# Performance work log

Measured on AMD Instinct MI355X. Metric: run time of the kernel, lower is better.

Reference implementation:

```python
import jax, jax.numpy as jnp
import numpy as np

B, D, HID, DC, K = 32768, 64, 512, 128, 12
CLAMP = 1.0
L1 = D // 2          # GLOW split lengths
L2 = D - L1
INIT = 0.01          # torch code rescales all params to 0.01*randn


def setup_inputs() -> dict:
    key = jax.random.key(0)
    ks = iter(jax.random.split(key, 16))
    # FrEIA PermuteRandom: np.random.seed(k); np.random.permutation(D)
    perms = jnp.asarray(
        np.stack([np.random.RandomState(k).permutation(D) for k in range(K)]),
        dtype=jnp.int32)
    f32 = jnp.float32
    return {
        'q_feat': jax.random.normal(next(ks), (B, 1, D), f32),
        'H': jax.random.normal(next(ks), (B, DC), f32),
        'perms': perms,
        'an_logscale': INIT * jax.random.normal(next(ks), (K, D), f32),
        'an_bias': INIT * jax.random.normal(next(ks), (K, D), f32),
        's1_W1': INIT * jax.random.normal(next(ks), (K, HID, L1 + DC), f32),
        's1_b1': INIT * jax.random.normal(next(ks), (K, HID), f32),
        's1_W2': INIT * jax.random.normal(next(ks), (K, 2 * L2, HID), f32),
        's1_b2': INIT * jax.random.normal(next(ks), (K, 2 * L2), f32),
        's2_W1': INIT * jax.random.normal(next(ks), (K, HID, L2 + DC), f32),
        's2_b1': INIT * jax.random.normal(next(ks), (K, HID), f32),
        's2_W2': INIT * jax.random.normal(next(ks), (K, 2 * L1, HID), f32),
        's2_b2': INIT * jax.random.normal(next(ks), (K, 2 * L1), f32),
    }


def _mlp(x, W1, b1, W2, b2):
    # torch Linear: y = x @ W.T + b
    h = jax.nn.relu(x @ W1.T + b1)
    return h @ W2.T + b2


def _log_e(s):
    # FrEIA GLOW soft clamp: log e(s) = clamp * 0.636 * atan(s / clamp)
    return CLAMP * 0.636 * jnp.arctan(s / CLAMP)


def reference(q_feat, H, perms, an_logscale, an_bias,
              s1_W1, s1_b1, s1_W2, s1_b2,
              s2_W1, s2_b1, s2_W2, s2_b2):
    x = q_feat.reshape(q_feat.shape[0], -1)          # Flatten: (B,1,D)->(B,D)
    logj = jnp.zeros(x.shape[0], x.dtype)

    def block(carry, p):
        x, logj = carry
        perm, ls, bi, w11, b11, w12, b12, w21, b21, w22, b22 = p
        x = x[:, perm]                               # PermuteRandom (logdet 0)
        x = x * jnp.exp(ls) + bi                     # ActNorm
        logj = logj + jnp.sum(ls)
        x1, x2 = x[:, :L1], x[:, L1:]                # GLOW coupling
        r2 = _mlp(jnp.concatenate([x2, H], 1), w21, b21, w22, b22)
        le2 = _log_e(r2[:, :L1])
        y1 = jnp.exp(le2) * x1 + r2[:, L1:]
        r1 = _mlp(jnp.concatenate([y1, H], 1), w11, b11, w12, b12)
        le1 = _log_e(r1[:, :L2])
        y2 = jnp.exp(le1) * x2 + r1[:, L2:]
        logj = logj + jnp.sum(le1, axis=1) + jnp.sum(le2, axis=1)
        return (jnp.concatenate([y1, y2], 1), logj), None

    (z, logj), _ = jax.lax.scan(
        block, (x, logj),
        (perms, an_logscale, an_bias,
         s1_W1, s1_b1, s1_W2, s1_b2,
         s2_W1, s2_b1, s2_W2, s2_b2))
    return z, logj
```

## Files before the change

### kernel.cpp

```cpp
#include <hip/hip_runtime.h>
#include <hip/hip_bf16.h>
#include <math.h>

#define B_ROWS 32768

typedef __attribute__((ext_vector_type(8)))  short        s8v;
typedef __attribute__((ext_vector_type(4)))  float        f4v;
typedef __attribute__((ext_vector_type(2)))  unsigned int u2v;
typedef __attribute__((ext_vector_type(4)))  unsigned int u4v;

__device__ __forceinline__ short f2bf(float f){
  unsigned u = __builtin_bit_cast(unsigned, f);
  u = (u + 0x7fffu + ((u >> 16) & 1u)) >> 16;
  return (short)u;
}
__device__ __forceinline__ unsigned cpk(float a, float b){
  __hip_bfloat16_raw lo = (__hip_bfloat16_raw)__float2bfloat16(a);
  __hip_bfloat16_raw hi = (__hip_bfloat16_raw)__float2bfloat16(b);
  return (unsigned)lo.x | ((unsigned)hi.x << 16);
}
__device__ __forceinline__ float bf_lo(unsigned u){ return __builtin_bit_cast(float, u << 16); }
__device__ __forceinline__ float bf_hi(unsigned u){ return __builtin_bit_cast(float, u & 0xffff0000u); }

#define MFMA16(A,B,C) __builtin_amdgcn_mfma_f32_16x16x32_bf16((A),(B),(C),0,0,0)

typedef __attribute__((address_space(1))) const unsigned int gu32;
typedef __attribute__((address_space(3))) unsigned int lu32;
__device__ __forceinline__ void gl_lds16(const unsigned short* g, char* l){
  __builtin_amdgcn_global_load_lds((gu32*)(const void*)g, (lu32*)(void*)l, 16, 0, 0);
}

#define OXFT 0
#define XFT_S 68
#define OXHB 17408
#define XHB_S 40
#define OHB  22528
#define HB_S 136
#define SL_S 68
#define SLOT_B 8704
#define OW1  39936
#define OLJ  80896
#define SM_SZ 81152

#define WF_W2 1966080
#define W_TOTAL 2752512

__global__ void cvtw_frag(const float* __restrict__ s1w1, const float* __restrict__ s1w2,
                          const float* __restrict__ s2w1, const float* __restrict__ s2w2,
                          unsigned short* __restrict__ dst)
{
  long t = (long)blockIdx.x * blockDim.x + threadIdx.x;
  if (t >= W_TOTAL) return;
  float v;
  if (t < WF_W2){
    int m = (int)(t / 81920); int r = (int)(t - (long)m*81920);
    int c = r / 20480;  int r2 = r - c*20480;
    int tile = r2 >> 9; int r3 = r2 & 511;
    int lane = r3 >> 3; int e = r3 & 7;
    int rg = tile / 5,  kk = tile - rg*5;
    int l15 = lane & 15, lq = lane >> 4;
    int h  = c*128 + rg*16 + l15;
    int ki = kk*32 + lq*8 + e;
    const float* src = (m & 1) ? s1w1 : s2w1;
    v = src[(size_t)(m >> 1)*81920 + h*160 + ki];
  } else {
    long u = t - WF_W2;
    int m = (int)(u / 32768); int r = (int)(u - (long)m*32768);
    int g = r >> 9; int r3 = r & 511;
    int lane = r3 >> 3; int e = r3 & 7;
    int c = g >> 4, hs = (g >> 2) & 3, ot = g & 3;
    int l15 = lane & 15, lq = lane >> 4;
    int o = ot*16 + l15;
    int h = c*128 + hs*32 + lq*8 + e;
    const float* src = (m & 1) ? s1w2 : s2w2;
    v = src[(size_t)(m >> 1)*32768 + o*512 + h];
  }
  dst[t] = (unsigned short)f2bf(v);
}

__global__ __launch_bounds__(256, 2) void cinn_dma(
    const float* __restrict__ q, const float* __restrict__ Hg,
    const int* __restrict__ perms,
    const float* __restrict__ ls_g, const float* __restrict__ bi_g,
    const float* __restrict__ s1b1, const float* __restrict__ s1b2,
    const float* __restrict__ s2b1, const float* __restrict__ s2b2,
    const unsigned short* __restrict__ wbf,
    float* __restrict__ outz, float* __restrict__ outlj)
{
  __shared__ __align__(16) char sm[SM_SZ];
  const int tid = threadIdx.x;
  const int rowbase = blockIdx.x * 64;
  const int lane = tid & 63, wave = tid >> 6;
  const int hw = wave >> 1, ng = wave & 1;
  const int l15 = lane & 15, lq = lane >> 4;

  float* XFT = (float*)(sm + OXFT);
  short* XHB = (short*)(sm + OXHB);
  short* HB  = (short*)(sm + OHB);
  float* LOGJ= (float*)(sm + OLJ);

  {
    int b = tid >> 2, j = tid & 3;
    const float* src = q + (size_t)(rowbase + b)*64 + j*16;
    #pragma unroll
    for (int i = 0; i < 4; ++i){
      f4v v = *(const f4v*)(src + 4*i);
      #pragma unroll
      for (int jj = 0; jj < 4; ++jj)
        XFT[(j*16 + 4*i + jj)*XFT_S + b] = v[jj];
    }
  }
  if (tid < 64) LOGJ[tid] = 0.f;
  __syncthreads();

  s8v hfr[2][4];
  #pragma unroll
  for (int nt = 0; nt < 2; ++nt){
    int b = rowbase + ng*32 + nt*16 + l15;
    #pragma unroll
    for (int kkh = 0; kkh < 4; ++kkh){
      const float* hp = Hg + (size_t)b*128 + kkh*32 + lq*8;
      f4v a = *(const f4v*)hp;
      f4v c = *(const f4v*)(hp + 4);
      u4v u = {cpk(a[0],a[1]), cpk(a[2],a[3]), cpk(c[0],c[1]), cpk(c[2],c[3])};
      hfr[nt][kkh] = __builtin_bit_cast(s8v, u);
    }
  }

  {
    const unsigned short* g = wbf + wave*5120 + lane*8;
    char* lb = sm + OW1 + wave*10240;
    #pragma unroll
    for (int k = 0; k < 10; ++k) gl_lds16(g + k*512, lb + k*1024);
  }

  for (int m = 0; m < 24; ++m){
    const int bp = m & 1;
    const unsigned short* w1sec = wbf + (size_t)m*81920;
    const unsigned short* w2sec = wbf + WF_W2 + (size_t)m*32768;
    const float* b1p = (bp ? s1b1 : s2b1) + (m >> 1)*512;
    const float* b2p = (bp ? s1b2 : s2b2) + (m >> 1)*64;

    if (!bp){
      int blk = m >> 1;
      int   pd = perms[blk*64 + lane];
      float e  = __expf(ls_g[blk*64 + lane]);
      float bi = bi_g[blk*64 + lane];
      int bg = wave;
      f4v v[4];
      #pragma unroll
      for (int i = 0; i < 4; ++i)
        v[i] = *(const f4v*)(XFT + pd*XFT_S + bg*16 + 4*i);
      __syncthreads();
      #pragma unroll
      for (int i = 0; i < 4; ++i){
        #pragma unroll
        for (int jj = 0; jj < 4; ++jj) v[i][jj] = fmaf(v[i][jj], e, bi);
        *(f4v*)(XFT + lane*XFT_S + bg*16 + 4*i) = v[i];
      }
      if (lane >= 32){
        #pragma unroll
        for (int i = 0; i < 4; ++i)
          #pragma unroll
          for (int jj = 0; jj < 4; ++jj)
            XHB[(bg*16 + 4*i + jj)*XHB_S + (lane - 32)] = f2bf(v[i][jj]);
      }
      __syncthreads();
    }

    s8v xk[2];
    #pragma unroll
    for (int nt = 0; nt < 2; ++nt)
      xk[nt] = *(const s8v*)(XHB + (ng*32 + nt*16 + l15)*XHB_S + lq*8);

    f4v b2v[4];
    if (hw == 0){
      #pragma unroll
      for (int ot = 0; ot < 4; ++ot)
        b2v[ot] = *(const f4v*)(b2p + ot*16 + lq*4);
    }

    f4v racc[4][2];
    #pragma unroll
    for (int ot = 0; ot < 4; ++ot)
      #pragma unroll
      for (int nt = 0; nt < 2; ++nt)
        racc[ot][nt] = (f4v){0.f,0.f,0.f,0.f};

    #pragma unroll
    for (int c = 0; c < 4; ++c){
      s8v w2c[2][4];
      #pragma unroll
      for (int kk2 = 0; kk2 < 2; ++kk2)
        #pragma unroll
        for (int ot = 0; ot < 4; ++ot)
          w2c[kk2][ot] = *(const s8v*)(w2sec + (size_t)((c*4 + hw*2 + kk2)*4 + ot)*512 + lane*8);
      f4v b1v[4];
      #pragma unroll
      for (int mt = 0; mt < 4; ++mt)
        b1v[mt] = *(const f4v*)(b1p + c*128 + hw*64 + mt*16 + lq*4);

      const short* W1c = (const short*)(sm + OW1);
      f4v acc[4][2];
      #pragma unroll
      for (int mt = 0; mt < 4; ++mt)
        #pragma unroll
        for (int nt = 0; nt < 2; ++nt) acc[mt][nt] = (f4v){0.f,0.f,0.f,0.f};
      #pragma unroll
      for (int kk = 0; kk < 5; ++kk){
        s8v a[4];
        #pragma unroll
        for (int mt = 0; mt < 4; ++mt)
          a[mt] = *(const s8v*)(W1c + ((hw*4 + mt)*5 + kk)*512 + lane*8);
        #pragma unroll
        for (int nt = 0; nt < 2; ++nt){
          s8v bb = (kk == 0) ? xk[nt] : hfr[nt][kk-1];
          #pragma unroll
          for (int mt = 0; mt < 4; ++mt)
            acc[mt][nt] = MFMA16(a[mt], bb, acc[mt][nt]);
        }
      }
      #pragma unroll
      for (int mt = 0; mt < 4; ++mt){
        f4v bv = b1v[mt];
        #pragma unroll
        for (int nt = 0; nt < 2; ++nt){
          float h0 = fmaxf(acc[mt][nt][0] + bv[0], 0.f);
          float h1 = fmaxf(acc[mt][nt][1] + bv[1], 0.f);
          float h2 = fmaxf(acc[mt][nt][2] + bv[2], 0.f);
          float h3 = fmaxf(acc[mt][nt][3] + bv[3], 0.f);
          *(u2v*)(HB + (ng*32 + nt*16 + l15)*HB_S + hw*64 + mt*16 + lq*4) = (u2v){cpk(h0,h1), cpk(h2,h3)};
        }
      }
      __syncthreads();

      if (!(m == 23 && c == 3)){
        const unsigned short* gsec = (c < 3) ? w1sec : (w1sec + 81920);
        const int cn = (c < 3) ? c + 1 : 0;
        const unsigned short* g = gsec + cn*20480 + wave*5120 + lane*8;
        char* lb = sm + OW1 + wave*10240;
        #pragma unroll
        for (int k = 0; k < 10; ++k) gl_lds16(g + k*512, lb + k*1024);
      }

      #pragma unroll
      for (int kk2 = 0; kk2 < 2; ++kk2){
        #pragma unroll
        for (int nt = 0; nt < 2; ++nt){
          s8v bb = *(const s8v*)(HB + (ng*32 + nt*16 + l15)*HB_S + hw*64 + kk2*32 + lq*8);
          #pragma unroll
          for (int ot = 0; ot < 4; ++ot)
            racc[ot][nt] = MFMA16(w2c[kk2][ot], bb, racc[ot][nt]);
        }
      }
      __syncthreads();
    }

    {
      short* SL = (short*)(sm + OHB + hw*SLOT_B);
      #pragma unroll
      for (int ot = 0; ot < 4; ++ot)
        #pragma unroll
        for (int nt = 0; nt < 2; ++nt){
          float r0 = racc[ot][nt][0], r1 = racc[ot][nt][1];
          float r2 = racc[ot][nt][2], r3 = racc[ot][nt][3];
          if (hw == 0){ r0 += b2v[ot][0]; r1 += b2v[ot][1]; r2 += b2v[ot][2]; r3 += b2v[ot][3]; }
          *(u2v*)(SL + (ng*32 + nt*16 + l15)*SL_S + ot*16 + lq*4) = (u2v){cpk(r0,r1), cpk(r2,r3)};
        }
    }
    __syncthreads();

    {
      int b = tid & 63, og = tid >> 6;
      float le[8] = {0,0,0,0,0,0,0,0}, ra[8] = {0,0,0,0,0,0,0,0};
      #pragma unroll
      for (int ms = 0; ms < 2; ++ms){
        const short* SL = (const short*)(sm + OHB + ms*SLOT_B);
        u2v L0 = *(const u2v*)(SL + b*SL_S + og*8);
        u2v L1 = *(const u2v*)(SL + b*SL_S + og*8 + 4);
        u2v R0 = *(const u2v*)(SL + b*SL_S + 32 + og*8);
        u2v R1 = *(const u2v*)(SL + b*SL_S + 32 + og*8 + 4);
        le[0]+=bf_lo(L0[0]); le[1]+=bf_hi(L0[0]); le[2]+=bf_lo(L0[1]); le[3]+=bf_hi(L0[1]);
        le[4]+=bf_lo(L1[0]); le[5]+=bf_hi(L1[0]); le[6]+=bf_lo(L1[1]); le[7]+=bf_hi(L1[1]);
        ra[0]+=bf_lo(R0[0]); ra[1]+=bf_hi(R0[0]); ra[2]+=bf_lo(R0[1]); ra[3]+=bf_hi(R0[1]);
        ra[4]+=bf_lo(R1[0]); ra[5]+=bf_hi(R1[0]); ra[6]+=bf_lo(R1[1]); ra[7]+=bf_hi(R1[1]);
      }
      float part = 0.f, y[8];
      #pragma unroll
      for (int j = 0; j < 8; ++j){
        float l = 0.636f * atanf(le[j]);
        int d = bp*32 + og*8 + j;
        y[j] = __expf(l) * XFT[d*XFT_S + b] + ra[j];
        XFT[d*XFT_S + b] = y[j];
        part += l;
      }
      if (!bp){
        u4v u = {cpk(y[0],y[1]), cpk(y[2],y[3]), cpk(y[4],y[5]), cpk(y[6],y[7])};
        *(u4v*)(XHB + b*XHB_S + og*8) = u;
      }
      atomicAdd(&LOGJ[b], part);
    }
    __syncthreads();
  }

  {
    int b = tid >> 2, j = tid & 3;
    float* dst = outz + (size_t)(rowbase + b)*64 + j*16;
    #pragma unroll
    for (int i = 0; i < 4; ++i){
      f4v w;
      #pragma unroll
      for (int jj = 0; jj < 4; ++jj)
        w[jj] = XFT[(j*16 + 4*i + jj)*XFT_S + b];
      *(f4v*)(dst + 4*i) = w;
    }
  }
  if (tid < 64){
    float p = 0.f;
    #pragma unroll
    for (int k = 0; k < 12; ++k) p += ls_g[k*64 + tid];
    #pragma unroll
    for (int off = 1; off < 64; off <<= 1) p += __shfl_xor(p, off);
    outlj[rowbase + tid] = LOGJ[tid] + p;
  }
}

extern "C" void kernel_launch(void* const* d_in, const int* in_sizes, int n_in,
                              void* d_out, int out_size, void* d_ws, size_t ws_size,
                              hipStream_t stream)
{
  const float* q    = (const float*)d_in[0];
  const float* Hg   = (const float*)d_in[1];
  const int*   perms= (const int*)  d_in[2];
  const float* ls   = (const float*)d_in[3];
  const float* bi   = (const float*)d_in[4];
  const float* s1W1 = (const float*)d_in[5];
  const float* s1b1 = (const float*)d_in[6];
  const float* s1W2 = (const float*)d_in[7];
  const float* s1b2 = (const float*)d_in[8];
  const float* s2W1 = (const float*)d_in[9];
  const float* s2b1 = (const float*)d_in[10];
  const float* s2W2 = (const float*)d_in[11];
  const float* s2b2 = (const float*)d_in[12];
  float* outz  = (float*)d_out;
  float* outlj = outz + (size_t)B_ROWS * 64;

  unsigned short* wbf = (unsigned short*)d_ws;
  cvtw_frag<<<2688, 1024, 0, stream>>>(s1W1, s1W2, s2W1, s2W2, wbf);
  cinn_dma<<<512, 256, 0, stream>>>(q, Hg, perms, ls, bi,
                                    s1b1, s1b2, s2b1, s2b2,
                                    wbf, outz, outlj);
}
```

Baseline: 272.5 us.

## Double-buffer W1 chunks in LDS with smaller hidden tiles and fast atan

Splits the hidden dimension into eight 64-wide chunks instead of four 128-wide ones. W1 chunks are double-buffered in LDS so the next chunk's DMA is issued at the top of each iteration. This lets one barrier per chunk replace two and lets the second MLP layer's MFMAs run right after the hidden activations are written. It also replaces atanf with a polynomial approximation. The costs are more loop iterations with less MFMA work per barrier, and slightly lower accuracy in the soft clamp.

```diff
diff --git a/kernel.cpp b/kernel.cpp
--- a/kernel.cpp
+++ b/kernel.cpp
@@ -21,6 +21,17 @@
 }
 __device__ __forceinline__ float bf_lo(unsigned u){ return __builtin_bit_cast(float, u << 16); }
 __device__ __forceinline__ float bf_hi(unsigned u){ return __builtin_bit_cast(float, u & 0xffff0000u); }
+
+__device__ __forceinline__ float atan_f(float t){
+  float a = fabsf(t);
+  bool big = a > 1.0f;
+  float u = big ? __builtin_amdgcn_rcpf(t) : t;
+  float s = u * u;
+  float p = fmaf(fmaf(fmaf(fmaf(s, 0.0208351f, -0.0851330f), s, 0.1801410f), s, -0.3302995f), s, 0.9998660f);
+  p = u * p;
+  float base = __builtin_copysignf(1.57079633f, t);
+  return big ? base - p : p;
+}
 
 #define MFMA16(A,B,C) __builtin_amdgcn_mfma_f32_16x16x32_bf16((A),(B),(C),0,0,0)
 
@@ -35,12 +46,13 @@
 #define OXHB 17408
 #define XHB_S 40
 #define OHB  22528
-#define HB_S 136
+#define HB_S 72
+#define OSL  31744
 #define SL_S 68
-#define SLOT_B 8704
-#define OW1  39936
-#define OLJ  80896
-#define SM_SZ 81152
+#define OW1  40448
+#define W1BUF 20480
+#define OLJ  81408
+#define SM_SZ 81664
 
 #define WF_W2 1966080
 #define W_TOTAL 2752512
@@ -54,12 +66,12 @@
   float v;
   if (t < WF_W2){
     int m = (int)(t / 81920); int r = (int)(t - (long)m*81920);
-    int c = r / 20480;  int r2 = r - c*20480;
+    int c = r / 10240;  int r2 = r - c*10240;
     int tile = r2 >> 9; int r3 = r2 & 511;
     int lane = r3 >> 3; int e = r3 & 7;
     int rg = tile / 5,  kk = tile - rg*5;
     int l15 = lane & 15, lq = lane >> 4;
-    int h  = c*128 + rg*16 + l15;
+    int h  = c*64 + rg*16 + l15;
     int ki = kk*32 + lq*8 + e;
     const float* src = (m & 1) ? s1w1 : s2w1;
     v = src[(size_t)(m >> 1)*81920 + h*160 + ki];
@@ -68,17 +80,17 @@
     int m = (int)(u / 32768); int r = (int)(u - (long)m*32768);
     int g = r >> 9; int r3 = r & 511;
     int lane = r3 >> 3; int e = r3 & 7;
-    int c = g >> 4, hs = (g >> 2) & 3, ot = g & 3;
+    int c = g >> 3, hs = (g >> 2) & 1, ot = g & 3;
     int l15 = lane & 15, lq = lane >> 4;
     int o = ot*16 + l15;
-    int h = c*128 + hs*32 + lq*8 + e;
+    int h = c*64 + hs*32 + lq*8 + e;
     const float* src = (m & 1) ? s1w2 : s2w2;
     v = src[(size_t)(m >> 1)*32768 + o*512 + h];
   }
   dst[t] = (unsigned short)f2bf(v);
 }
 
-__global__ __launch_bounds__(256, 2) void cinn_dma(
+__global__ __launch_bounds__(256, 2) void cinn_dma2(
     const float* __restrict__ q, const float* __restrict__ Hg,
     const int* __restrict__ perms,
     const float* __restrict__ ls_g, const float* __restrict__ bi_g,
@@ -128,10 +140,10 @@
   }
 
   {
-    const unsigned short* g = wbf + wave*5120 + lane*8;
-    char* lb = sm + OW1 + wave*10240;
-    #pragma unroll
-    for (int k = 0; k < 10; ++k) gl_lds16(g + k*512, lb + k*1024);
+    const unsigned short* g = wbf + wave*2560 + lane*8;
+    char* lb = sm + OW1 + wave*5120;
+    #pragma unroll
+    for (int k = 0; k < 5; ++k) gl_lds16(g + k*512, lb + k*1024);
   }
 
   for (int m = 0; m < 24; ++m){
@@ -188,76 +200,63 @@
         racc[ot][nt] = (f4v){0.f,0.f,0.f,0.f};
 
     #pragma unroll
-    for (int c = 0; c < 4; ++c){
-      s8v w2c[2][4];
-      #pragma unroll
-      for (int kk2 = 0; kk2 < 2; ++kk2)
-        #pragma unroll
-        for (int ot = 0; ot < 4; ++ot)
-          w2c[kk2][ot] = *(const s8v*)(w2sec + (size_t)((c*4 + hw*2 + kk2)*4 + ot)*512 + lane*8);
-      f4v b1v[4];
-      #pragma unroll
-      for (int mt = 0; mt < 4; ++mt)
-        b1v[mt] = *(const f4v*)(b1p + c*128 + hw*64 + mt*16 + lq*4);
-
-      const short* W1c = (const short*)(sm + OW1);
-      f4v acc[4][2];
-      #pragma unroll
-      for (int mt = 0; mt < 4; ++mt)
+    for (int c = 0; c < 8; ++c){
+      if (!(m == 23 && c == 7)){
+        const unsigned short* gsec = (c < 7) ? w1sec : (w1sec + 81920);
+        const int cn = (c < 7) ? c + 1 : 0;
+        const unsigned short* g = gsec + cn*10240 + wave*2560 + lane*8;
+        char* lb = sm + OW1 + ((c+1)&1)*W1BUF + wave*5120;
+        #pragma unroll
+        for (int k = 0; k < 5; ++k) gl_lds16(g + k*512, lb + k*1024);
+      }
+      s8v w2c[4];
+      #pragma unroll
+      for (int ot = 0; ot < 4; ++ot)
+        w2c[ot] = *(const s8v*)(w2sec + (size_t)((c*2 + hw)*4 + ot)*512 + lane*8);
+      f4v b1v0 = *(const f4v*)(b1p + c*64 + hw*32 + lq*4);
+      f4v b1v1 = *(const f4v*)(b1p + c*64 + hw*32 + 16 + lq*4);
+
+      const short* W1c = (const short*)(sm + OW1 + (c&1)*W1BUF);
+      f4v acc[2][2];
+      #pragma unroll
+      for (int mt = 0; mt < 2; ++mt)
         #pragma unroll
         for (int nt = 0; nt < 2; ++nt) acc[mt][nt] = (f4v){0.f,0.f,0.f,0.f};
       #pragma unroll
       for (int kk = 0; kk < 5; ++kk){
-        s8v a[4];
-        #pragma unroll
-        for (int mt = 0; mt < 4; ++mt)
-          a[mt] = *(const s8v*)(W1c + ((hw*4 + mt)*5 + kk)*512 + lane*8);
+        s8v a0 = *(const s8v*)(W1c + ((hw*2 + 0)*5 + kk)*512 + lane*8);
+        s8v a1 = *(const s8v*)(W1c + ((hw*2 + 1)*5 + kk)*512 + lane*8);
         #pragma unroll
         for (int nt = 0; nt < 2; ++nt){
           s8v bb = (kk == 0) ? xk[nt] : hfr[nt][kk-1];
-          #pragma unroll
-          for (int mt = 0; mt < 4; ++mt)
-            acc[mt][nt] = MFMA16(a[mt], bb, acc[mt][nt]);
+          acc[0][nt] = MFMA16(a0, bb, acc[0][nt]);
+          acc[1][nt] = MFMA16(a1, bb, acc[1][nt]);
         }
       }
       #pragma unroll
-      for (int mt = 0; mt < 4; ++mt){
-        f4v bv = b1v[mt];
+      for (int mt = 0; mt < 2; ++mt){
+        f4v bv = mt ? b1v1 : b1v0;
         #pragma unroll
         for (int nt = 0; nt < 2; ++nt){
           float h0 = fmaxf(acc[mt][nt][0] + bv[0], 0.f);
           float h1 = fmaxf(acc[mt][nt][1] + bv[1], 0.f);
           float h2 = fmaxf(acc[mt][nt][2] + bv[2], 0.f);
           float h3 = fmaxf(acc[mt][nt][3] + bv[3], 0.f);
-          *(u2v*)(HB + (ng*32 + nt*16 + l15)*HB_S + hw*64 + mt*16 + lq*4) = (u2v){cpk(h0,h1), cpk(h2,h3)};
+          *(u2v*)(HB + (ng*32 + nt*16 + l15)*HB_S + hw*32 + mt*16 + lq*4) = (u2v){cpk(h0,h1), cpk(h2,h3)};
         }
       }
+      #pragma unroll
+      for (int nt = 0; nt < 2; ++nt){
+        s8v bb = *(const s8v*)(HB + (ng*32 + nt*16 + l15)*HB_S + hw*32 + lq*8);
+        #pragma unroll
+        for (int ot = 0; ot < 4; ++ot)
+          racc[ot][nt] = MFMA16(w2c[ot], bb, racc[ot][nt]);
+      }
       __syncthreads();
-
-      if (!(m == 23 && c == 3)){
-        const unsigned short* gsec = (c < 3) ? w1sec : (w1sec + 81920);
-        const int cn = (c < 3) ? c + 1 : 0;
-        const unsigned short* g = gsec + cn*20480 + wave*5120 + lane*8;
-        char* lb = sm + OW1 + wave*10240;
-        #pragma unroll
-        for (int k = 0; k < 10; ++k) gl_lds16(g + k*512, lb + k*1024);
-      }
-
-      #pragma unroll
-      for (int kk2 = 0; kk2 < 2; ++kk2){
-        #pragma unroll
-        for (int nt = 0; nt < 2; ++nt){
-          s8v bb = *(const s8v*)(HB + (ng*32 + nt*16 + l15)*HB_S + hw*64 + kk2*32 + lq*8);
-          #pragma unroll
-          for (int ot = 0; ot < 4; ++ot)
-            racc[ot][nt] = MFMA16(w2c[kk2][ot], bb, racc[ot][nt]);
-        }
-      }
-      __syncthreads();
     }
 
     {
-      short* SL = (short*)(sm + OHB + hw*SLOT_B);
+      short* SL = (hw == 0) ? (short*)(sm + OSL) : (short*)(sm + OHB);
       #pragma unroll
       for (int ot = 0; ot < 4; ++ot)
         #pragma unroll
@@ -275,7 +274,7 @@
       float le[8] = {0,0,0,0,0,0,0,0}, ra[8] = {0,0,0,0,0,0,0,0};
       #pragma unroll
       for (int ms = 0; ms < 2; ++ms){
-        const short* SL = (const short*)(sm + OHB + ms*SLOT_B);
+        const short* SL = (ms == 0) ? (const short*)(sm + OSL) : (const short*)(sm + OHB);
         u2v L0 = *(const u2v*)(SL + b*SL_S + og*8);
         u2v L1 = *(const u2v*)(SL + b*SL_S + og*8 + 4);
         u2v R0 = *(const u2v*)(SL + b*SL_S + 32 + og*8);
@@ -288,7 +287,7 @@
       float part = 0.f, y[8];
       #pragma unroll
       for (int j = 0; j < 8; ++j){
-        float l = 0.636f * atanf(le[j]);
+        float l = 0.636f * atan_f(le[j]);
         int d = bp*32 + og*8 + j;
         y[j] = __expf(l) * XFT[d*XFT_S + b] + ra[j];
         XFT[d*XFT_S + b] = y[j];
@@ -347,7 +346,7 @@
 
   unsigned short* wbf = (unsigned short*)d_ws;
   cvtw_frag<<<2688, 1024, 0, stream>>>(s1W1, s1W2, s2W1, s2W2, wbf);
-  cinn_dma<<<512, 256, 0, stream>>>(q, Hg, perms, ls, bi,
-                                    s1b1, s1b2, s2b1, s2b2,
-                                    wbf, outz, outlj);
-}
+  cinn_dma2<<<512, 256, 0, stream>>>(q, Hg, perms, ls, bi,
+                                     s1b1, s1b2, s2b1, s2b2,
+                                     wbf, outz, outlj);
+}
```

New measurement: 273.1 us. No clear change (+0.2%).
